# Performance work log

Measured on AMD Instinct MI355X. Metric: run time of the kernel, lower is better.

Reference implementation:

```python
import jax, jax.numpy as jnp
import numpy as np

H = 128          # h_dim
F_IN = 3 * H     # leaf/edge feature dim
N = 65536        # number of center nodes
E = 1000000      # number of leaf nodes / edges


def setup_inputs() -> dict:
    key = jax.random.key(0)
    ks = jax.random.split(key, 8)
    center_node_attr = jax.random.normal(ks[0], (N, H), jnp.float32)
    leaf_node_all = jax.random.normal(ks[1], (E, F_IN), jnp.float32)
    node_idx = jax.random.randint(ks[2], (E,), 0, N, dtype=jnp.int32)
    gcnfeats = jax.random.normal(ks[3], (N, H), jnp.float32)
    # nn.Linear default init: U(-1/sqrt(fan_in), 1/sqrt(fan_in))
    s1 = 1.0 / np.sqrt(F_IN)
    s2 = 1.0 / np.sqrt(H)
    W1 = jax.random.uniform(ks[4], (F_IN, H), jnp.float32, -s1, s1)
    b1 = jax.random.uniform(ks[5], (H,), jnp.float32, -s1, s1)
    W2 = jax.random.uniform(ks[6], (H, H), jnp.float32, -s2, s2)
    b2 = jax.random.uniform(ks[7], (H,), jnp.float32, -s2, s2)
    return dict(center_node_attr=center_node_attr, leaf_node_all=leaf_node_all,
                node_idx=node_idx, gcnfeats=gcnfeats, W1=W1, b1=b1, W2=W2, b2=b2)


def reference(center_node_attr, leaf_node_all, node_idx, gcnfeats, W1, b1, W2, b2):
    # per-edge 2-layer MLP message: encoder(x_j)  [E, H]
    msg = jax.nn.relu(leaf_node_all @ W1 + b1) @ W2 + b2
    # scatter-max aggregation into center nodes (PyG aggr='max'); empty nodes -> 0
    neg = jnp.finfo(msg.dtype).min
    agg = jnp.full(center_node_attr.shape, neg, msg.dtype).at[node_idx].max(msg)
    agg = jnp.where(agg == neg, jnp.zeros((), msg.dtype), agg)
    lang_gcnfeats = center_node_attr + agg  # [N, H]
    # cosine similarity along dim=1 (torch eps=1e-8 clamps each norm)
    eps = 1e-8
    na = jnp.maximum(jnp.linalg.norm(gcnfeats, axis=1), eps)
    nb = jnp.maximum(jnp.linalg.norm(lang_gcnfeats, axis=1), eps)
    return jnp.sum(gcnfeats * lang_gcnfeats, axis=1) / (na * nb)  # [N]
```

## Files before the change

### kernel.cpp

```cpp
#include <hip/hip_runtime.h>

#define H_DIM 128
#define F_IN  384

typedef __bf16 v8bf __attribute__((ext_vector_type(8)));
typedef float  v4f  __attribute__((ext_vector_type(4)));

__device__ __forceinline__ unsigned enc_f32(float v) {
    unsigned u = __float_as_uint(v);
    return (u & 0x80000000u) ? ~u : (u | 0x80000000u);
}
__device__ __forceinline__ float dec_f32(unsigned e) {
    if (e == 0u) return 0.0f;
    unsigned u = (e & 0x80000000u) ? (e & 0x7fffffffu) : ~e;
    return __uint_as_float(u);
}

__global__ __launch_bounds__(256) void wconvert(const float* __restrict__ W1,
                                                const float* __restrict__ W2,
                                                __bf16* __restrict__ W1T,
                                                __bf16* __restrict__ W2T) {
    int i = blockIdx.x * 256 + threadIdx.x;
    if (i < F_IN * H_DIM) {
        int col = i / F_IN, k = i % F_IN;
        W1T[i] = (__bf16)W1[k * H_DIM + col];
    } else if (i < F_IN * H_DIM + H_DIM * H_DIM) {
        int j = i - F_IN * H_DIM;
        int col = j / H_DIM, k = j % H_DIM;
        W2T[j] = (__bf16)W2[k * H_DIM + col];
    }
}

__global__ __launch_bounds__(256) void mlp_scatter(
    const float* __restrict__ leaf, const int* __restrict__ nidx,
    const __bf16* __restrict__ W1T, const __bf16* __restrict__ W2T,
    const float* __restrict__ b1, const float* __restrict__ b2,
    unsigned* __restrict__ agg, int E)
{
    __shared__ __bf16 wb[2][128][40];
    __shared__ __bf16 hs[128][136];
    __shared__ int   idx_s[128];
    __shared__ float b1_s[H_DIM], b2_s[H_DIM];

    const int t  = threadIdx.x;
    const int w  = t >> 6;
    const int l  = t & 63;
    const int lr = l & 15;
    const int lg = l >> 4;
    const long e0 = (long)blockIdx.x * 128;

    if (t < 128) {
        long e = e0 + t;
        idx_s[t] = nidx[e < E ? e : (E - 1)];
    }
    if (t < H_DIM) { b1_s[t] = b1[t]; b2_s[t] = b2[t]; }

    {
        const int col = t >> 1, kh = (t & 1) * 16;
        const v8bf* src = (const v8bf*)(W1T + col * F_IN + kh);
        *(v8bf*)&wb[0][col][kh]     = src[0];
        *(v8bf*)&wb[0][col][kh + 8] = src[1];
    }

    long erA = e0 + w * 32 + lr;
    long erB = e0 + w * 32 + 16 + lr;
    if (erA >= E) erA = E - 1;
    if (erB >= E) erB = E - 1;
    const float* arowA = leaf + erA * (long)F_IN + lg * 8;
    const float* arowB = leaf + erB * (long)F_IN + lg * 8;

    const v4f vzero = {0.f, 0.f, 0.f, 0.f};
    v4f accA[8], accB[8];
#pragma unroll
    for (int f = 0; f < 8; ++f) { accA[f] = vzero; accB[f] = vzero; }

    float4 aA0 = *(const float4*)(arowA);
    float4 aA1 = *(const float4*)(arowA + 4);
    float4 aB0 = *(const float4*)(arowB);
    float4 aB1 = *(const float4*)(arowB + 4);
    __syncthreads();

    for (int ks = 0; ks < 12; ++ks) {
        float4 nA0 = aA0, nA1 = aA1, nB0 = aB0, nB1 = aB1;
        if (ks + 1 < 12) {
            nA0 = *(const float4*)(arowA + (ks + 1) * 32);
            nA1 = *(const float4*)(arowA + (ks + 1) * 32 + 4);
            nB0 = *(const float4*)(arowB + (ks + 1) * 32);
            nB1 = *(const float4*)(arowB + (ks + 1) * 32 + 4);
            const int col = t >> 1, kh = (t & 1) * 16;
            const v8bf* src = (const v8bf*)(W1T + col * F_IN + (ks + 1) * 32 + kh);
            const int b = (ks + 1) & 1;
            *(v8bf*)&wb[b][col][kh]     = src[0];
            *(v8bf*)&wb[b][col][kh + 8] = src[1];
        }
        v8bf afA, afB;
        afA[0] = (__bf16)aA0.x; afA[1] = (__bf16)aA0.y; afA[2] = (__bf16)aA0.z; afA[3] = (__bf16)aA0.w;
        afA[4] = (__bf16)aA1.x; afA[5] = (__bf16)aA1.y; afA[6] = (__bf16)aA1.z; afA[7] = (__bf16)aA1.w;
        afB[0] = (__bf16)aB0.x; afB[1] = (__bf16)aB0.y; afB[2] = (__bf16)aB0.z; afB[3] = (__bf16)aB0.w;
        afB[4] = (__bf16)aB1.x; afB[5] = (__bf16)aB1.y; afB[6] = (__bf16)aB1.z; afB[7] = (__bf16)aB1.w;
        const int cb = ks & 1;
#pragma unroll
        for (int f = 0; f < 8; ++f) {
            v8bf bfv = *(const v8bf*)&wb[cb][f * 16 + lr][lg * 8];
            accA[f] = __builtin_amdgcn_mfma_f32_16x16x32_bf16(afA, bfv, accA[f], 0, 0, 0);
            accB[f] = __builtin_amdgcn_mfma_f32_16x16x32_bf16(afB, bfv, accB[f], 0, 0, 0);
        }
        aA0 = nA0; aA1 = nA1; aB0 = nB0; aB1 = nB1;
        __syncthreads();
    }

#pragma unroll
    for (int f = 0; f < 8; ++f) {
        const float bb = b1_s[f * 16 + lr];
#pragma unroll
        for (int j = 0; j < 4; ++j) {
            float vA = fmaxf(accA[f][j] + bb, 0.0f);
            float vB = fmaxf(accB[f][j] + bb, 0.0f);
            hs[w * 32 + lg * 4 + j][f * 16 + lr]      = (__bf16)vA;
            hs[w * 32 + 16 + lg * 4 + j][f * 16 + lr] = (__bf16)vB;
        }
    }
    __syncthreads();

    v4f acc2A[8], acc2B[8];
#pragma unroll
    for (int f = 0; f < 8; ++f) { acc2A[f] = vzero; acc2B[f] = vzero; }
#pragma unroll
    for (int ks = 0; ks < 4; ++ks) {
        v8bf afA2 = *(const v8bf*)&hs[w * 32 + lr][ks * 32 + lg * 8];
        v8bf afB2 = *(const v8bf*)&hs[w * 32 + 16 + lr][ks * 32 + lg * 8];
#pragma unroll
        for (int f = 0; f < 8; ++f) {
            v8bf bfv = *(const v8bf*)(W2T + (f * 16 + lr) * H_DIM + ks * 32 + lg * 8);
            acc2A[f] = __builtin_amdgcn_mfma_f32_16x16x32_bf16(afA2, bfv, acc2A[f], 0, 0, 0);
            acc2B[f] = __builtin_amdgcn_mfma_f32_16x16x32_bf16(afB2, bfv, acc2B[f], 0, 0, 0);
        }
    }

#pragma unroll
    for (int g = 0; g < 2; ++g) {
        const int rb = w * 32 + g * 16 + lg * 4;
#pragma unroll
        for (int j = 0; j < 4; ++j) {
            const long ej = e0 + rb + j;
            if (ej < E) {
                const int node = idx_s[rb + j];
                unsigned* dst = agg + (long)node * H_DIM + lr;
#pragma unroll
                for (int f = 0; f < 8; ++f) {
                    float v = (g ? acc2B[f][j] : acc2A[f][j]) + b2_s[f * 16 + lr];
                    atomicMax(dst + f * 16, enc_f32(v));
                }
            }
        }
    }
}

__global__ __launch_bounds__(256) void cos_kernel(
    const float* __restrict__ center, const float* __restrict__ gcn,
    const unsigned* __restrict__ agg, float* __restrict__ out, int N)
{
    const int w = threadIdx.x >> 6, l = threadIdx.x & 63;
    const long row = (long)blockIdx.x * 4 + w;
    if (row >= N) return;
    const float2 g2 = *(const float2*)(gcn    + row * H_DIM + l * 2);
    const float2 c2 = *(const float2*)(center + row * H_DIM + l * 2);
    const uint2  e2 = *(const uint2*) (agg    + row * H_DIM + l * 2);
    const float l0 = c2.x + dec_f32(e2.x);
    const float l1 = c2.y + dec_f32(e2.y);
    float sgl = g2.x * l0 + g2.y * l1;
    float sgg = g2.x * g2.x + g2.y * g2.y;
    float sll = l0 * l0 + l1 * l1;
#pragma unroll
    for (int off = 32; off; off >>= 1) {
        sgl += __shfl_xor(sgl, off);
        sgg += __shfl_xor(sgg, off);
        sll += __shfl_xor(sll, off);
    }
    if (l == 0) {
        const float na = fmaxf(sqrtf(sgg), 1e-8f);
        const float nb = fmaxf(sqrtf(sll), 1e-8f);
        out[row] = sgl / (na * nb);
    }
}

extern "C" void kernel_launch(void* const* d_in, const int* in_sizes, int n_in,
                              void* d_out, int out_size, void* d_ws, size_t ws_size,
                              hipStream_t stream) {
    const float* center = (const float*)d_in[0];
    const float* leaf   = (const float*)d_in[1];
    const int*   nidx   = (const int*)  d_in[2];
    const float* gcn    = (const float*)d_in[3];
    const float* W1     = (const float*)d_in[4];
    const float* b1     = (const float*)d_in[5];
    const float* W2     = (const float*)d_in[6];
    const float* b2     = (const float*)d_in[7];

    const int E = in_sizes[2];
    const int N = in_sizes[0] / H_DIM;

    unsigned* agg = (unsigned*)d_ws;
    const size_t aggBytes = (size_t)N * H_DIM * sizeof(unsigned);
    __bf16* W1T = (__bf16*)((char*)d_ws + aggBytes);
    __bf16* W2T = W1T + (size_t)F_IN * H_DIM;

    hipMemsetAsync(agg, 0, aggBytes, stream);
    wconvert<<<(F_IN * H_DIM + H_DIM * H_DIM + 255) / 256, 256, 0, stream>>>(W1, W2, W1T, W2T);
    mlp_scatter<<<(E + 127) / 128, 256, 0, stream>>>(leaf, nidx, W1T, W2T, b1, b2, agg, E);
    cos_kernel<<<(N + 3) / 4, 256, 0, stream>>>(center, gcn, agg, (float*)d_out, N);
}
```

Measured before the change: 657.2 us.

## Stage all of W1 into LDS upfront and drop per-step barriers

Pre-arranges W1 into k-slice-major bf16 chunks. Each block loads the whole W1 into shared memory once, instead of double-buffering one 32-wide k slice per step. This removes the __syncthreads in every k step and the barrier before the hidden-layer readback, which is safe because each wave reads only its own hs rows. The cost is about 155KB of LDS per block, which limits each CU to one block and weakens latency hiding on the large leaf-feature stream.

```diff
diff --git a/kernel.cpp b/kernel.cpp
--- a/kernel.cpp
+++ b/kernel.cpp
@@ -18,12 +18,12 @@
 
 __global__ __launch_bounds__(256) void wconvert(const float* __restrict__ W1,
                                                 const float* __restrict__ W2,
-                                                __bf16* __restrict__ W1T,
+                                                __bf16* __restrict__ W1C,
                                                 __bf16* __restrict__ W2T) {
     int i = blockIdx.x * 256 + threadIdx.x;
     if (i < F_IN * H_DIM) {
-        int col = i / F_IN, k = i % F_IN;
-        W1T[i] = (__bf16)W1[k * H_DIM + col];
+        int ks = i >> 12, rem = i & 4095, col = rem >> 5, kk = rem & 31;
+        W1C[i] = (__bf16)W1[(ks * 32 + kk) * H_DIM + col];
     } else if (i < F_IN * H_DIM + H_DIM * H_DIM) {
         int j = i - F_IN * H_DIM;
         int col = j / H_DIM, k = j % H_DIM;
@@ -33,11 +33,11 @@
 
 __global__ __launch_bounds__(256) void mlp_scatter(
     const float* __restrict__ leaf, const int* __restrict__ nidx,
-    const __bf16* __restrict__ W1T, const __bf16* __restrict__ W2T,
+    const __bf16* __restrict__ W1C, const __bf16* __restrict__ W2T,
     const float* __restrict__ b1, const float* __restrict__ b2,
     unsigned* __restrict__ agg, int E)
 {
-    __shared__ __bf16 wb[2][128][40];
+    __shared__ __bf16 w1s[12][128][40];
     __shared__ __bf16 hs[128][136];
     __shared__ int   idx_s[128];
     __shared__ float b1_s[H_DIM], b2_s[H_DIM];
@@ -56,10 +56,19 @@
     if (t < H_DIM) { b1_s[t] = b1[t]; b2_s[t] = b2[t]; }
 
     {
-        const int col = t >> 1, kh = (t & 1) * 16;
-        const v8bf* src = (const v8bf*)(W1T + col * F_IN + kh);
-        *(v8bf*)&wb[0][col][kh]     = src[0];
-        *(v8bf*)&wb[0][col][kh + 8] = src[1];
+        const int colt = t >> 1, kht = (t & 1) * 16;
+        v8bf s0[12], s1[12];
+#pragma unroll
+        for (int ks = 0; ks < 12; ++ks) {
+            const v8bf* src = (const v8bf*)(W1C + ks * 4096 + colt * 32 + kht);
+            s0[ks] = src[0];
+            s1[ks] = src[1];
+        }
+#pragma unroll
+        for (int ks = 0; ks < 12; ++ks) {
+            *(v8bf*)&w1s[ks][colt][kht]     = s0[ks];
+            *(v8bf*)&w1s[ks][colt][kht + 8] = s1[ks];
+        }
     }
 
     long erA = e0 + w * 32 + lr;
@@ -80,6 +89,7 @@
     float4 aB1 = *(const float4*)(arowB + 4);
     __syncthreads();
 
+#pragma unroll
     for (int ks = 0; ks < 12; ++ks) {
         float4 nA0 = aA0, nA1 = aA1, nB0 = aB0, nB1 = aB1;
         if (ks + 1 < 12) {
@@ -87,26 +97,19 @@
             nA1 = *(const float4*)(arowA + (ks + 1) * 32 + 4);
             nB0 = *(const float4*)(arowB + (ks + 1) * 32);
             nB1 = *(const float4*)(arowB + (ks + 1) * 32 + 4);
-            const int col = t >> 1, kh = (t & 1) * 16;
-            const v8bf* src = (const v8bf*)(W1T + col * F_IN + (ks + 1) * 32 + kh);
-            const int b = (ks + 1) & 1;
-            *(v8bf*)&wb[b][col][kh]     = src[0];
-            *(v8bf*)&wb[b][col][kh + 8] = src[1];
         }
         v8bf afA, afB;
         afA[0] = (__bf16)aA0.x; afA[1] = (__bf16)aA0.y; afA[2] = (__bf16)aA0.z; afA[3] = (__bf16)aA0.w;
         afA[4] = (__bf16)aA1.x; afA[5] = (__bf16)aA1.y; afA[6] = (__bf16)aA1.z; afA[7] = (__bf16)aA1.w;
         afB[0] = (__bf16)aB0.x; afB[1] = (__bf16)aB0.y; afB[2] = (__bf16)aB0.z; afB[3] = (__bf16)aB0.w;
         afB[4] = (__bf16)aB1.x; afB[5] = (__bf16)aB1.y; afB[6] = (__bf16)aB1.z; afB[7] = (__bf16)aB1.w;
-        const int cb = ks & 1;
 #pragma unroll
         for (int f = 0; f < 8; ++f) {
-            v8bf bfv = *(const v8bf*)&wb[cb][f * 16 + lr][lg * 8];
+            v8bf bfv = *(const v8bf*)&w1s[ks][f * 16 + lr][lg * 8];
             accA[f] = __builtin_amdgcn_mfma_f32_16x16x32_bf16(afA, bfv, accA[f], 0, 0, 0);
             accB[f] = __builtin_amdgcn_mfma_f32_16x16x32_bf16(afB, bfv, accB[f], 0, 0, 0);
         }
         aA0 = nA0; aA1 = nA1; aB0 = nB0; aB1 = nB1;
-        __syncthreads();
     }
 
 #pragma unroll
@@ -120,7 +123,6 @@
             hs[w * 32 + 16 + lg * 4 + j][f * 16 + lr] = (__bf16)vB;
         }
     }
-    __syncthreads();
 
     v4f acc2A[8], acc2B[8];
 #pragma unroll
@@ -201,11 +203,11 @@
 
     unsigned* agg = (unsigned*)d_ws;
     const size_t aggBytes = (size_t)N * H_DIM * sizeof(unsigned);
-    __bf16* W1T = (__bf16*)((char*)d_ws + aggBytes);
-    __bf16* W2T = W1T + (size_t)F_IN * H_DIM;
+    __bf16* W1C = (__bf16*)((char*)d_ws + aggBytes);
+    __bf16* W2T = W1C + (size_t)F_IN * H_DIM;
 
     hipMemsetAsync(agg, 0, aggBytes, stream);
-    wconvert<<<(F_IN * H_DIM + H_DIM * H_DIM + 255) / 256, 256, 0, stream>>>(W1, W2, W1T, W2T);
-    mlp_scatter<<<(E + 127) / 128, 256, 0, stream>>>(leaf, nidx, W1T, W2T, b1, b2, agg, E);
+    wconvert<<<(F_IN * H_DIM + H_DIM * H_DIM + 255) / 256, 256, 0, stream>>>(W1, W2, W1C, W2T);
+    mlp_scatter<<<(E + 127) / 128, 256, 0, stream>>>(leaf, nidx, W1C, W2T, b1, b2, agg, E);
     cos_kernel<<<(N + 3) / 4, 256, 0, stream>>>(center, gcn, agg, (float*)d_out, N);
 }
```

After: 848.8 us. +29.2%, slower.
